# Kernel tuning notes

Measured on AMD Instinct MI355X. Metric: run time of the kernel, lower is better.

Reference implementation:

```python
import jax, jax.numpy as jnp
import numpy as np
import math

D_MODEL = 512
N_HEADS = 8
FACTOR = 5
B, L = 2, 2048


def setup_inputs() -> dict:
    key = jax.random.key(0)
    ks = jax.random.split(key, 10)
    s = 1.0 / math.sqrt(D_MODEL)
    inp = {
        "x": jax.random.normal(ks[0], (B, L, D_MODEL), dtype=jnp.float32),
        "samp_idx": jax.random.randint(ks[1], (FACTOR * L,), 0, L),
        "Wq": jax.random.normal(ks[2], (D_MODEL, D_MODEL), dtype=jnp.float32) * s,
        "bq": jnp.zeros((D_MODEL,), dtype=jnp.float32),
        "Wk": jax.random.normal(ks[3], (D_MODEL, D_MODEL), dtype=jnp.float32) * s,
        "bk": jnp.zeros((D_MODEL,), dtype=jnp.float32),
        "Wv": jax.random.normal(ks[4], (D_MODEL, D_MODEL), dtype=jnp.float32) * s,
        "bv": jnp.zeros((D_MODEL,), dtype=jnp.float32),
        "Wo": jax.random.normal(ks[5], (D_MODEL, D_MODEL), dtype=jnp.float32) * s,
        "bo": jnp.zeros((D_MODEL,), dtype=jnp.float32),
    }
    return inp


def reference(x, Wq, bq, Wk, bk, Wv, bv, Wo, bo, samp_idx):
    B_, L_, D = x.shape
    H = N_HEADS
    dk = D // H
    scale = 1.0 / math.sqrt(dk)

    def proj(W, b):
        # torch Linear: x @ W.T + b, then split heads -> [B, H, L, dk]
        y = jnp.einsum('bld,ed->ble', x, W) + b
        return y.reshape(B_, L_, H, dk).transpose(0, 2, 1, 3)

    q = proj(Wq, bq)
    k = proj(Wk, bk)
    v = proj(Wv, bv)

    # _prob_QK: random key sampling (shared indices across B, H)
    K_sample = k[:, :, samp_idx, :]                       # [B, H, factor*L, dk]
    QKs = jnp.einsum('bhle,bhse->bhls', q, K_sample) * scale  # [B, H, L, factor*L]
    M = QKs.max(-1) - QKs.mean(-1)                        # [B, H, L]
    U = jnp.argmax(M, axis=-1)                            # [B, H] -- single query per head

    # gather the selected query per (b, h): [B, H, 1, dk]
    q_red = jnp.take_along_axis(q, U[:, :, None, None], axis=2)

    scores = jnp.einsum('bhle,bhse->bhls', q_red, k) * scale  # [B, H, 1, L]
    attn = jax.nn.softmax(scores, axis=-1)
    context = jnp.einsum('bhls,bhse->bhle', attn, v)          # [B, H, 1, dk]

    # expand to all query positions, merge heads
    context = jnp.broadcast_to(context, (B_, H, L_, dk))
    context = context.transpose(0, 2, 1, 3).reshape(B_, L_, D)
    return jnp.einsum('bld,ed->ble', context, Wo) + bo
```

## Files before the change

### kernel.cpp

```cpp
#include <hip/hip_runtime.h>

#define B_ 2
#define L_ 2048
#define D_ 512
#define H_ 8
#define DK 64
#define S_ 10240
#define SCALE 0.125f
#define MP_SLICES 16

#define QSZ (4096 * 512)

typedef _Float16 f16;
typedef __attribute__((ext_vector_type(8))) _Float16 f16x8;
typedef __attribute__((ext_vector_type(4))) float f32x4;

__global__ __launch_bounds__(256) void split_x_kernel(
    const float* __restrict__ x, f16* __restrict__ xh, f16* __restrict__ xl)
{
    const size_t i0 = ((size_t)blockIdx.x * 256 + threadIdx.x) * 8;
    const float4 a = *(const float4*)&x[i0];
    const float4 b = *(const float4*)&x[i0 + 4];
    const float vals[8] = {a.x, a.y, a.z, a.w, b.x, b.y, b.z, b.w};
    union { f16 h[8]; uint4 u; } H, Lo;
#pragma unroll
    for (int j = 0; j < 8; j++) {
        const f16 hh = (f16)vals[j];
        H.h[j] = hh;
        Lo.h[j] = (f16)(vals[j] - (float)hh);
    }
    *(uint4*)&xh[i0] = H.u;
    *(uint4*)&xl[i0] = Lo.u;
}

__global__ __launch_bounds__(256) void split_w_kernel(
    const float* __restrict__ Wq, const float* __restrict__ Wk,
    const float* __restrict__ bq, const float* __restrict__ bk,
    f16* __restrict__ wh, f16* __restrict__ wl, float* __restrict__ biascat)
{
    const size_t i0 = ((size_t)blockIdx.x * 256 + threadIdx.x) * 8;
    const float* src = (i0 < (size_t)512 * 512) ? Wq + i0 : Wk + (i0 - (size_t)512 * 512);
    const float4 a = *(const float4*)&src[0];
    const float4 b = *(const float4*)&src[4];
    const float vals[8] = {a.x, a.y, a.z, a.w, b.x, b.y, b.z, b.w};
    union { f16 h[8]; uint4 u; } H, Lo;
#pragma unroll
    for (int j = 0; j < 8; j++) {
        const f16 hh = (f16)vals[j];
        H.h[j] = hh;
        Lo.h[j] = (f16)(vals[j] - (float)hh);
    }
    *(uint4*)&wh[i0] = H.u;
    *(uint4*)&wl[i0] = Lo.u;
    if (blockIdx.x == 0)
        for (int e = threadIdx.x; e < 1024; e += 256)
            biascat[e] = (e < 512) ? bq[e] : bk[e - 512];
}

__global__ __launch_bounds__(256) void projqk_kernel(
    const f16* __restrict__ xh, const f16* __restrict__ xl,
    const f16* __restrict__ wh, const f16* __restrict__ wl,
    const float* __restrict__ biascat,
    f16* __restrict__ qh, f16* __restrict__ ql,
    f16* __restrict__ kh, f16* __restrict__ kl)
{
    const int n0 = blockIdx.x * 128;
    const int e0 = blockIdx.y * 128;
    const int t = threadIdx.x;

    __shared__ __align__(16) f16 lds[4 * 128 * 64];
    f16* ash = lds;
    f16* asl = lds + 8192;
    f16* bsh = lds + 16384;
    f16* bsl = lds + 24576;

    const int lane = t & 63, wid = t >> 6;
    const int wr = wid >> 1, wc = wid & 1;
    const int lrow = lane & 15, lk = lane >> 4;

    f32x4 acc[4][4];
#pragma unroll
    for (int i = 0; i < 4; i++)
#pragma unroll
        for (int j = 0; j < 4; j++)
#pragma unroll
            for (int r = 0; r < 4; r++) acc[i][j][r] = 0.f;

    for (int kt = 0; kt < 8; kt++) {
        __syncthreads();
#pragma unroll
        for (int i = 0; i < 4; i++) {
            const int g = i * 256 + t;
            const int row = g >> 3, c = g & 7;
            const int cs = c ^ (row & 7);
            const int lo = row * 64 + cs * 8;
            const size_t ga = (size_t)(n0 + row) * 512 + kt * 64 + c * 8;
            const size_t gb = (size_t)(e0 + row) * 512 + kt * 64 + c * 8;
            *(uint4*)&ash[lo] = *(const uint4*)&xh[ga];
            *(uint4*)&asl[lo] = *(const uint4*)&xl[ga];
            *(uint4*)&bsh[lo] = *(const uint4*)&wh[gb];
            *(uint4*)&bsl[lo] = *(const uint4*)&wl[gb];
        }
        __syncthreads();

#pragma unroll
        for (int kk = 0; kk < 2; kk++) {
            f16x8 ah[4], al[4], bh_[4], bl_[4];
#pragma unroll
            for (int lt = 0; lt < 4; lt++) {
                const int row = wr * 64 + lt * 16 + lrow;
                const int cs = (kk * 4 + lk) ^ (row & 7);
                const int o = row * 64 + cs * 8;
                ah[lt] = *(const f16x8*)&ash[o];
                al[lt] = *(const f16x8*)&asl[o];
            }
#pragma unroll
            for (int jt = 0; jt < 4; jt++) {
                const int row = wc * 64 + jt * 16 + lrow;
                const int cs = (kk * 4 + lk) ^ (row & 7);
                const int o = row * 64 + cs * 8;
                bh_[jt] = *(const f16x8*)&bsh[o];
                bl_[jt] = *(const f16x8*)&bsl[o];
            }
#pragma unroll
            for (int lt = 0; lt < 4; lt++)
#pragma unroll
                for (int jt = 0; jt < 4; jt++) {
                    acc[lt][jt] = __builtin_amdgcn_mfma_f32_16x16x32_f16(
                        ah[lt], bh_[jt], acc[lt][jt], 0, 0, 0);
                    acc[lt][jt] = __builtin_amdgcn_mfma_f32_16x16x32_f16(
                        ah[lt], bl_[jt], acc[lt][jt], 0, 0, 0);
                    acc[lt][jt] = __builtin_amdgcn_mfma_f32_16x16x32_f16(
                        al[lt], bh_[jt], acc[lt][jt], 0, 0, 0);
                }
        }
    }

    const int PSTR = 72;
    f16* tile = lds + wid * 64 * PSTR;
    const int ebase = e0 + wc * 64;
    const bool isQ = (blockIdx.y < 4);
    const int colbase = (blockIdx.y & 3) * 128;

#pragma unroll
    for (int round = 0; round < 2; round++) {
        __syncthreads();
#pragma unroll
        for (int jt = 0; jt < 4; jt++) {
            const float bval = biascat[ebase + jt * 16 + lrow];
#pragma unroll
            for (int lt = 0; lt < 4; lt++)
#pragma unroll
                for (int r = 0; r < 4; r++) {
                    const float y = acc[lt][jt][r] + bval;
                    const f16 hi = (f16)y;
                    const f16 val = (round == 0) ? hi : (f16)(y - (float)hi);
                    tile[(lt * 16 + lk * 4 + r) * PSTR + jt * 16 + lrow] = val;
                }
        }
        __syncthreads();
        f16* dst = isQ ? ((round == 0) ? qh : ql) : ((round == 0) ? kh : kl);
        for (int i = t; i < 2048; i += 256) {
            const int w = i >> 9, rem = i & 511, row = rem >> 3, c = rem & 7;
            const int n = n0 + (w >> 1) * 64 + row;
            const int col = colbase + (w & 1) * 64 + c * 8;
            *(uint4*)&dst[(size_t)n * 512 + col] =
                *(const uint4*)&lds[w * 64 * PSTR + row * PSTR + c * 8];
        }
    }
}

__global__ void hist_kernel(const int* __restrict__ samp, int* __restrict__ counts)
{
    const int i = blockIdx.x * 256 + threadIdx.x;
    if (i < S_) atomicAdd(&counts[samp[i]], 1);
}

__global__ __launch_bounds__(256) void kbar_part_kernel(
    const f16* __restrict__ kh, const f16* __restrict__ kl,
    const int* __restrict__ counts, float* __restrict__ kbar_part)
{
    const int bh = blockIdx.x, c = blockIdx.y;
    const int b = bh >> 3, h = bh & 7;
    const int j0 = c * 256;
    const int t = threadIdx.x;
    const int e = t & 63, jg = t >> 6;
    const f16* kbh = kh + (size_t)b * L_ * D_ + h * DK + e;
    const f16* kbl = kl + (size_t)b * L_ * D_ + h * DK + e;
    float s = 0.f;
    for (int j = j0 + jg; j < j0 + 256; j += 4) {
        const float kv = (float)kbh[(size_t)j * D_] + (float)kbl[(size_t)j * D_];
        s += (float)counts[j] * kv;
    }
    __shared__ float red[4][64];
    red[jg][e] = s;
    __syncthreads();
    if (t < 64)
        kbar_part[(size_t)(bh * 8 + c) * 64 + t] =
            red[0][t] + red[1][t] + red[2][t] + red[3][t];
}

__global__ __launch_bounds__(256) void mstat_kernel(
    const f16* __restrict__ qh, const f16* __restrict__ ql,
    const f16* __restrict__ kh, const f16* __restrict__ kl,
    const int* __restrict__ counts, float* __restrict__ Mpart)
{
    const int lt16 = blockIdx.x;
    const int bh   = blockIdx.y;
    const int jt16 = blockIdx.z;
    const int b = bh >> 3, h = bh & 7;
    const int l0 = lt16 * 128, j0 = jt16 * 128;
    const int t = threadIdx.x;

    __shared__ __align__(16) f16 qsh[128 * 64];
    __shared__ __align__(16) f16 qsl[128 * 64];
    __shared__ __align__(16) f16 ksh[128 * 64];
    __shared__ __align__(16) f16 ksl[128 * 64];

    {
        const size_t qbase = (size_t)(b * L_ + l0) * D_ + h * DK;
        const size_t kbase = (size_t)(b * L_ + j0) * D_ + h * DK;
#pragma unroll
        for (int i = 0; i < 4; i++) {
            const int g = i * 256 + t;
            const int row = g >> 3, c = g & 7;
            const int cs = c ^ (row & 7);
            const size_t go = (size_t)row * D_ + c * 8;
            const int lo = row * 64 + cs * 8;
            *(uint4*)&qsh[lo] = *(const uint4*)&qh[qbase + go];
            *(uint4*)&qsl[lo] = *(const uint4*)&ql[qbase + go];
            *(uint4*)&ksh[lo] = *(const uint4*)&kh[kbase + go];
            *(uint4*)&ksl[lo] = *(const uint4*)&kl[kbase + go];
        }
    }
    __syncthreads();

    const int lane = t & 63, wid = t >> 6;
    const int wr = wid >> 1, wc = wid & 1;
    const int lrow = lane & 15, lk = lane >> 4;

    f32x4 acc[4][4];
#pragma unroll
    for (int i = 0; i < 4; i++)
#pragma unroll
        for (int j = 0; j < 4; j++)
#pragma unroll
            for (int r = 0; r < 4; r++) acc[i][j][r] = 0.f;

#pragma unroll
    for (int kk = 0; kk < 2; kk++) {
        f16x8 ah[4], al[4], bh_[4], bl_[4];
#pragma unroll
        for (int lt = 0; lt < 4; lt++) {
            const int row = wr * 64 + lt * 16 + lrow;
            const int cs = (kk * 4 + lk) ^ (row & 7);
            const int o = row * 64 + cs * 8;
            ah[lt] = *(const f16x8*)&qsh[o];
            al[lt] = *(const f16x8*)&qsl[o];
        }
#pragma unroll
        for (int jt = 0; jt < 4; jt++) {
            const int row = wc * 64 + jt * 16 + lrow;
            const int cs = (kk * 4 + lk) ^ (row & 7);
            const int o = row * 64 + cs * 8;
            bh_[jt] = *(const f16x8*)&ksh[o];
            bl_[jt] = *(const f16x8*)&ksl[o];
        }
#pragma unroll
        for (int lt = 0; lt < 4; lt++)
#pragma unroll
            for (int jt = 0; jt < 4; jt++) {
                acc[lt][jt] = __builtin_amdgcn_mfma_f32_16x16x32_f16(
                    ah[lt], bh_[jt], acc[lt][jt], 0, 0, 0);
                acc[lt][jt] = __builtin_amdgcn_mfma_f32_16x16x32_f16(
                    ah[lt], bl_[jt], acc[lt][jt], 0, 0, 0);
                acc[lt][jt] = __builtin_amdgcn_mfma_f32_16x16x32_f16(
                    al[lt], bh_[jt], acc[lt][jt], 0, 0, 0);
            }
    }

    float rmax[4][4];
#pragma unroll
    for (int lt = 0; lt < 4; lt++)
#pragma unroll
        for (int r = 0; r < 4; r++) rmax[lt][r] = -3.9e38f;

#pragma unroll
    for (int jt = 0; jt < 4; jt++) {
        const int cj = j0 + wc * 64 + jt * 16 + lrow;
        const float addend = (counts[cj] > 0) ? 0.f : -3.0e38f;
#pragma unroll
        for (int lt = 0; lt < 4; lt++)
#pragma unroll
            for (int r = 0; r < 4; r++)
                rmax[lt][r] = fmaxf(rmax[lt][r], acc[lt][jt][r] + addend);
    }

#pragma unroll
    for (int m = 1; m < 16; m <<= 1)
#pragma unroll
        for (int lt = 0; lt < 4; lt++)
#pragma unroll
            for (int r = 0; r < 4; r++)
                rmax[lt][r] = fmaxf(rmax[lt][r], __shfl_xor(rmax[lt][r], m));

    __syncthreads();
    float* wred = (float*)qsh;
    if (lrow == 0) {
#pragma unroll
        for (int lt = 0; lt < 4; lt++)
#pragma unroll
            for (int r = 0; r < 4; r++)
                wred[wc * 128 + wr * 64 + lt * 16 + lk * 4 + r] = rmax[lt][r];
    }
    __syncthreads();
    if (t < 128)
        Mpart[(size_t)(jt16 * 16 + bh) * L_ + l0 + t] =
            fmaxf(wred[t], wred[128 + t]);
}

__global__ __launch_bounds__(256) void argmax1_kernel(
    const f16* __restrict__ qh, const f16* __restrict__ ql,
    const float* __restrict__ kbar_part, const float* __restrict__ Mpart,
    float* __restrict__ bestv, int* __restrict__ besti)
{
    const int bh = blockIdx.x, c = blockIdx.y;
    const int b = bh >> 3, h = bh & 7;
    const int l0 = c * 256;
    const int t = threadIdx.x;

    __shared__ float kb[64];
    if (t < 64) {
        float s = 0.f;
#pragma unroll
        for (int p = 0; p < 8; p++) s += kbar_part[(size_t)(bh * 8 + p) * 64 + t];
        kb[t] = s * (1.0f / (float)S_);
    }
    __syncthreads();

    const int l = l0 + t;
    const f16* qrh = qh + (size_t)(b * L_ + l) * D_ + h * DK;
    const f16* qrl = ql + (size_t)(b * L_ + l) * D_ + h * DK;
    float dot = 0.f;
#pragma unroll
    for (int cc = 0; cc < 8; cc++) {
        const f16x8 hv = *(const f16x8*)&qrh[cc * 8];
        const f16x8 lv = *(const f16x8*)&qrl[cc * 8];
#pragma unroll
        for (int i = 0; i < 8; i++)
            dot += ((float)hv[i] + (float)lv[i]) * kb[cc * 8 + i];
    }
    float mx = Mpart[(size_t)(0 * 16 + bh) * L_ + l];
#pragma unroll
    for (int p = 1; p < MP_SLICES; p++)
        mx = fmaxf(mx, Mpart[(size_t)(p * 16 + bh) * L_ + l]);
    const float val = mx - dot;

    __shared__ float bvs[256];
    __shared__ int bis[256];
    bvs[t] = val; bis[t] = l;
    __syncthreads();
    for (int s = 128; s > 0; s >>= 1) {
        if (t < s) {
            const float ov = bvs[t + s]; const int oi = bis[t + s];
            if (ov > bvs[t] || (ov == bvs[t] && oi < bis[t])) { bvs[t] = ov; bis[t] = oi; }
        }
        __syncthreads();
    }
    if (t == 0) { bestv[bh * 8 + c] = bvs[0]; besti[bh * 8 + c] = bis[0]; }
}

__global__ void argmax2_kernel(const float* __restrict__ bestv,
                               const int* __restrict__ besti, int* __restrict__ U)
{
    const int t = threadIdx.x;
    if (t < 16) {
        float best = -3.9e38f;
        int bi = 0;
#pragma unroll
        for (int c = 0; c < 8; c++) {
            const float v = bestv[t * 8 + c];
            if (v > best) { best = v; bi = besti[t * 8 + c]; }
        }
        U[t] = bi;
    }
}

__global__ __launch_bounds__(256) void ctx_part_kernel(
    const f16* __restrict__ qh, const f16* __restrict__ ql,
    const f16* __restrict__ kh, const f16* __restrict__ kl,
    const float* __restrict__ x, const int* __restrict__ U,
    float* __restrict__ xbar_part, float* __restrict__ cm, float* __restrict__ cs)
{
    const int bh = blockIdx.x, c = blockIdx.y;
    const int b = bh >> 3, h = bh & 7;
    const int l0 = c * 128;
    const int t = threadIdx.x;

    __shared__ float qr[64];
    __shared__ float w[128];
    __shared__ float red[128];

    const int u = U[bh];
    if (t < 64)
        qr[t] = (float)qh[(size_t)(b * L_ + u) * D_ + h * DK + t] +
                (float)ql[(size_t)(b * L_ + u) * D_ + h * DK + t];
    __syncthreads();

    {
        const int row = t >> 1, half = t & 1;
        const size_t off = (size_t)(b * L_ + l0 + row) * D_ + h * DK + half * 32;
        const f16* krh = kh + off;
        const f16* krl = kl + off;
        float dot = 0.f;
#pragma unroll
        for (int cc = 0; cc < 4; cc++) {
            const f16x8 hv = *(const f16x8*)&krh[cc * 8];
            const f16x8 lv = *(const f16x8*)&krl[cc * 8];
#pragma unroll
            for (int i = 0; i < 8; i++)
                dot += ((float)hv[i] + (float)lv[i]) * qr[half * 32 + cc * 8 + i];
        }
        dot += __shfl_xor(dot, 1);
        if (half == 0) w[row] = dot * SCALE;
    }
    __syncthreads();

    if (t < 128) red[t] = w[t];
    __syncthreads();
    for (int s = 64; s > 0; s >>= 1) {
        if (t < s) red[t] = fmaxf(red[t], red[t + s]);
        __syncthreads();
    }
    const float m = red[0];
    __syncthreads();

    if (t < 128) { const float e = expf(w[t] - m); w[t] = e; red[t] = e; }
    __syncthreads();
    for (int s = 64; s > 0; s >>= 1) {
        if (t < s) red[t] += red[t + s];
        __syncthreads();
    }
    const float ssum = red[0];

    float ax = 0.f, ay = 0.f;
    const float* xb = x + (size_t)(b * L_ + l0) * D_ + t * 2;
#pragma unroll 4
    for (int l = 0; l < 128; l++) {
        const float wl = w[l];
        const float2 xv = *(const float2*)(xb + (size_t)l * D_);
        ax = fmaf(wl, xv.x, ax);
        ay = fmaf(wl, xv.y, ay);
    }
    float2 st; st.x = ax; st.y = ay;
    *(float2*)&xbar_part[(size_t)(bh * 16 + c) * 512 + t * 2] = st;
    if (t == 0) { cm[bh * 16 + c] = m; cs[bh * 16 + c] = ssum; }
}

__global__ __launch_bounds__(256) void ctx_combine_kernel(
    const float* __restrict__ xbar_part, const float* __restrict__ cm,
    const float* __restrict__ cs, const float* __restrict__ Wv,
    const float* __restrict__ bv, float* __restrict__ ctx)
{
    const int bh = blockIdx.x;
    const int h = bh & 7;
    const int t = threadIdx.x;
    __shared__ float xbar[512];

    float M = -3.9e38f;
#pragma unroll
    for (int c = 0; c < 16; c++) M = fmaxf(M, cm[bh * 16 + c]);
    float denom = 0.f;
    float ax = 0.f, ay = 0.f;
#pragma unroll
    for (int c = 0; c < 16; c++) {
        const float f = expf(cm[bh * 16 + c] - M);
        denom += f * cs[bh * 16 + c];
        const float2 p = *(const float2*)&xbar_part[(size_t)(bh * 16 + c) * 512 + t * 2];
        ax = fmaf(f, p.x, ax);
        ay = fmaf(f, p.y, ay);
    }
    xbar[t * 2] = ax; xbar[t * 2 + 1] = ay;
    __syncthreads();

    if (t < 64) {
        const float* wr = Wv + (size_t)(h * 64 + t) * D_;
        float acc = 0.f;
#pragma unroll 8
        for (int d = 0; d < 128; d++) {
            const float4 wv4 = *(const float4*)&wr[d * 4];
            acc += wv4.x * xbar[d * 4] + wv4.y * xbar[d * 4 + 1] +
                   wv4.z * xbar[d * 4 + 2] + wv4.w * xbar[d * 4 + 3];
        }
        ctx[bh * 64 + t] = acc / denom + bv[h * 64 + t];
    }
}

__global__ __launch_bounds__(256) void out_kernel(
    const float* __restrict__ ctx, const float* __restrict__ Wo,
    const float* __restrict__ bo, float* __restrict__ out)
{
    const int b = blockIdx.x;
    const int sl = blockIdx.y;
    const int t = threadIdx.x;
    __shared__ float cb[512];
    __shared__ float row[512];

    cb[t] = ctx[b * 512 + t];
    cb[t + 256] = ctx[b * 512 + 256 + t];
    __syncthreads();

#pragma unroll
    for (int r = 0; r < 2; r++) {
        const int e = t + r * 256;
        const float* wr = Wo + (size_t)e * D_;
        float acc = 0.f;
#pragma unroll 8
        for (int c = 0; c < 128; c++) {
            const float4 wv = *(const float4*)(wr + c * 4);
            acc += wv.x * cb[c * 4] + wv.y * cb[c * 4 + 1] +
                   wv.z * cb[c * 4 + 2] + wv.w * cb[c * 4 + 3];
        }
        row[e] = acc + bo[e];
    }
    __syncthreads();

    const float4* r4 = (const float4*)row;
    float4* o4 = (float4*)(out + ((size_t)b * L_ + sl * 32) * D_);
    for (int i = t; i < 32 * 128; i += 256) {
        const int l = i >> 7, c = i & 127;
        o4[l * 128 + c] = r4[c];
    }
}

extern "C" void kernel_launch(void* const* d_in, const int* in_sizes, int n_in,
                              void* d_out, int out_size, void* d_ws, size_t ws_size,
                              hipStream_t stream)
{
    const float* x   = (const float*)d_in[0];
    const int* samp  = (const int*)d_in[1];
    const float* Wq  = (const float*)d_in[2];
    const float* bq  = (const float*)d_in[3];
    const float* Wk  = (const float*)d_in[4];
    const float* bk  = (const float*)d_in[5];
    const float* Wv  = (const float*)d_in[6];
    const float* bv  = (const float*)d_in[7];
    const float* Wo  = (const float*)d_in[8];
    const float* bo  = (const float*)d_in[9];
    float* out = (float*)d_out;

    f16* qh = (f16*)d_ws;
    f16* ql = qh + QSZ;
    f16* kh = ql + QSZ;
    f16* kl = kh + QSZ;
    f16* xh = kl + QSZ;
    f16* xl = xh + QSZ;
    f16* wh = xl + QSZ;
    f16* wl = wh + 1024 * 512;
    float* fbase     = (float*)(wl + 1024 * 512);
    float* biascat   = fbase;
    float* Mpart     = biascat + 1024;
    float* kbar_part = Mpart + MP_SLICES * 16 * L_;
    float* xbar_part = kbar_part + 8192;
    float* cm        = xbar_part + 131072;
    float* cs        = cm + 256;
    float* bestv     = cs + 256;
    float* ctx       = bestv + 128;
    int* counts      = (int*)(ctx + 1024);
    int* besti       = counts + 2048;
    int* U           = besti + 128;

    hipMemsetAsync(counts, 0, 2048 * sizeof(int), stream);
    split_x_kernel<<<1024, 256, 0, stream>>>(x, xh, xl);
    split_w_kernel<<<256, 256, 0, stream>>>(Wq, Wk, bq, bk, wh, wl, biascat);
    projqk_kernel<<<dim3(32, 8), 256, 0, stream>>>(xh, xl, wh, wl, biascat,
                                                   qh, ql, kh, kl);
    hist_kernel<<<40, 256, 0, stream>>>(samp, counts);
    kbar_part_kernel<<<dim3(16, 8), 256, 0, stream>>>(kh, kl, counts, kbar_part);
    mstat_kernel<<<dim3(16, 16, 16), 256, 0, stream>>>(qh, ql, kh, kl, counts, Mpart);
    argmax1_kernel<<<dim3(16, 8), 256, 0, stream>>>(qh, ql, kbar_part, Mpart, bestv, besti);
    argmax2_kernel<<<1, 64, 0, stream>>>(bestv, besti, U);
    ctx_part_kernel<<<dim3(16, 16), 256, 0, stream>>>(qh, ql, kh, kl, x, U,
                                                      xbar_part, cm, cs);
    ctx_combine_kernel<<<16, 256, 0, stream>>>(xbar_part, cm, cs, Wv, bv, ctx);
    out_kernel<<<dim3(2, 64), 256, 0, stream>>>(ctx, Wo, bo, out);
}
```

Before: 164.8 us.

## Fuse M-statistic and argmax into persistent-over-keys mstat kernel with double-buffered K tiles

The mstat kernel now has each block loop over all 16 key tiles, with double-buffered LDS staging. It keeps the query fragments in registers and folds the max reduction, the kbar dot product and the per-block argmax into the same kernel. This removes the Mpart global round trip, the argmax1 kernel and the j-slice grid dimension, and it remaps block IDs so blocks for the same head land on the same XCD. The output stage is split into a tiny row-compute kernel and a wide broadcast kernel, so the Wo matvec is no longer repeated 64 times. The trade-off is that the grid drops from 4096 blocks to 256 longer-running blocks and two extra launches are added.

Result: slower. 206.0 us (+25.0%).

```diff
diff --git a/kernel.cpp b/kernel.cpp
--- a/kernel.cpp
+++ b/kernel.cpp
@@ -7,7 +7,6 @@
 #define DK 64
 #define S_ 10240
 #define SCALE 0.125f
-#define MP_SLICES 16
 
 #define QSZ (4096 * 512)
 
@@ -200,84 +199,76 @@
             red[0][t] + red[1][t] + red[2][t] + red[3][t];
 }
 
+__global__ void kbar_combine_kernel(const float* __restrict__ kbar_part,
+                                    float* __restrict__ kbar)
+{
+    const int bh = blockIdx.x;
+    const int t = threadIdx.x;
+    float s = 0.f;
+#pragma unroll
+    for (int p = 0; p < 8; p++) s += kbar_part[(size_t)(bh * 8 + p) * 64 + t];
+    kbar[bh * 64 + t] = s * (1.0f / (float)S_);
+}
+
 __global__ __launch_bounds__(256) void mstat_kernel(
     const f16* __restrict__ qh, const f16* __restrict__ ql,
     const f16* __restrict__ kh, const f16* __restrict__ kl,
-    const int* __restrict__ counts, float* __restrict__ Mpart)
-{
-    const int lt16 = blockIdx.x;
-    const int bh   = blockIdx.y;
-    const int jt16 = blockIdx.z;
+    const int* __restrict__ counts, const float* __restrict__ kbar,
+    float* __restrict__ bestv, int* __restrict__ besti)
+{
+    const int id = blockIdx.x;
+    const int xcd = id & 7, seq = id >> 3;
+    const int bh = xcd * 2 + (seq >> 4);
+    const int lt16 = seq & 15;
     const int b = bh >> 3, h = bh & 7;
-    const int l0 = lt16 * 128, j0 = jt16 * 128;
-    const int t = threadIdx.x;
-
-    __shared__ __align__(16) f16 qsh[128 * 64];
-    __shared__ __align__(16) f16 qsl[128 * 64];
-    __shared__ __align__(16) f16 ksh[128 * 64];
-    __shared__ __align__(16) f16 ksl[128 * 64];
-
-    {
-        const size_t qbase = (size_t)(b * L_ + l0) * D_ + h * DK;
-        const size_t kbase = (size_t)(b * L_ + j0) * D_ + h * DK;
-#pragma unroll
-        for (int i = 0; i < 4; i++) {
-            const int g = i * 256 + t;
-            const int row = g >> 3, c = g & 7;
-            const int cs = c ^ (row & 7);
-            const size_t go = (size_t)row * D_ + c * 8;
-            const int lo = row * 64 + cs * 8;
-            *(uint4*)&qsh[lo] = *(const uint4*)&qh[qbase + go];
-            *(uint4*)&qsl[lo] = *(const uint4*)&ql[qbase + go];
-            *(uint4*)&ksh[lo] = *(const uint4*)&kh[kbase + go];
-            *(uint4*)&ksl[lo] = *(const uint4*)&kl[kbase + go];
-        }
-    }
-    __syncthreads();
-
+    const int l0 = lt16 * 128;
+    const int t = threadIdx.x;
     const int lane = t & 63, wid = t >> 6;
     const int wr = wid >> 1, wc = wid & 1;
     const int lrow = lane & 15, lk = lane >> 4;
 
-    f32x4 acc[4][4];
-#pragma unroll
-    for (int i = 0; i < 4; i++)
-#pragma unroll
-        for (int j = 0; j < 4; j++)
-#pragma unroll
-            for (int r = 0; r < 4; r++) acc[i][j][r] = 0.f;
-
-#pragma unroll
-    for (int kk = 0; kk < 2; kk++) {
-        f16x8 ah[4], al[4], bh_[4], bl_[4];
-#pragma unroll
-        for (int lt = 0; lt < 4; lt++) {
-            const int row = wr * 64 + lt * 16 + lrow;
-            const int cs = (kk * 4 + lk) ^ (row & 7);
-            const int o = row * 64 + cs * 8;
-            ah[lt] = *(const f16x8*)&qsh[o];
-            al[lt] = *(const f16x8*)&qsl[o];
-        }
-#pragma unroll
-        for (int jt = 0; jt < 4; jt++) {
-            const int row = wc * 64 + jt * 16 + lrow;
-            const int cs = (kk * 4 + lk) ^ (row & 7);
-            const int o = row * 64 + cs * 8;
-            bh_[jt] = *(const f16x8*)&ksh[o];
-            bl_[jt] = *(const f16x8*)&ksl[o];
-        }
-#pragma unroll
-        for (int lt = 0; lt < 4; lt++)
-#pragma unroll
-            for (int jt = 0; jt < 4; jt++) {
-                acc[lt][jt] = __builtin_amdgcn_mfma_f32_16x16x32_f16(
-                    ah[lt], bh_[jt], acc[lt][jt], 0, 0, 0);
-                acc[lt][jt] = __builtin_amdgcn_mfma_f32_16x16x32_f16(
-                    ah[lt], bl_[jt], acc[lt][jt], 0, 0, 0);
-                acc[lt][jt] = __builtin_amdgcn_mfma_f32_16x16x32_f16(
-                    al[lt], bh_[jt], acc[lt][jt], 0, 0, 0);
+    __shared__ __align__(16) f16 kbuf[2][2][128 * 64];
+    __shared__ float kbar_lds[64];
+    __shared__ float dot_lds[128];
+    __shared__ float wv_[4];
+    __shared__ int wi_[4];
+
+    f16x8 qa_h[2][4], qa_l[2][4];
+    {
+        const size_t qrowbase = (size_t)(b * L_ + l0 + wr * 64) * D_ + h * DK;
+#pragma unroll
+        for (int kk = 0; kk < 2; kk++)
+#pragma unroll
+            for (int lt = 0; lt < 4; lt++) {
+                const size_t o = qrowbase + (size_t)(lt * 16 + lrow) * D_ + kk * 32 + lk * 8;
+                qa_h[kk][lt] = *(const f16x8*)&qh[o];
+                qa_l[kk][lt] = *(const f16x8*)&ql[o];
             }
     }
+    if (t < 64) kbar_lds[t] = kbar[bh * 64 + t];
+
+    const f16* khb = kh + (size_t)b * L_ * D_ + h * DK;
+    const f16* klb = kl + (size_t)b * L_ * D_ + h * DK;
+
+    const int srow = t >> 3, sc = t & 7;
+    (void)srow; (void)sc;
+
+    uint4 rh[4], rl[4];
+#pragma unroll
+    for (int i = 0; i < 4; i++) {
+        const int g = i * 256 + t, row = g >> 3, c = g & 7;
+        const size_t go = (size_t)row * D_ + c * 8;
+        rh[i] = *(const uint4*)&khb[go];
+        rl[i] = *(const uint4*)&klb[go];
+    }
+#pragma unroll
+    for (int i = 0; i < 4; i++) {
+        const int g = i * 256 + t, row = g >> 3, c = g & 7;
+        const int cs = c ^ (row & 7);
+        *(uint4*)&kbuf[0][0][row * 64 + cs * 8] = rh[i];
+        *(uint4*)&kbuf[0][1][row * 64 + cs * 8] = rl[i];
+    }
+    __syncthreads();
 
     float rmax[4][4];
 #pragma unroll
@@ -285,15 +276,74 @@
 #pragma unroll
         for (int r = 0; r < 4; r++) rmax[lt][r] = -3.9e38f;
 
-#pragma unroll
-    for (int jt = 0; jt < 4; jt++) {
-        const int cj = j0 + wc * 64 + jt * 16 + lrow;
-        const float addend = (counts[cj] > 0) ? 0.f : -3.0e38f;
-#pragma unroll
-        for (int lt = 0; lt < 4; lt++)
-#pragma unroll
-            for (int r = 0; r < 4; r++)
-                rmax[lt][r] = fmaxf(rmax[lt][r], acc[lt][jt][r] + addend);
+    int cur = 0;
+    for (int jt = 0; jt < 16; jt++) {
+        if (jt < 15) {
+            const size_t kbase = (size_t)((jt + 1) * 128) * D_;
+#pragma unroll
+            for (int i = 0; i < 4; i++) {
+                const int g = i * 256 + t, row = g >> 3, c = g & 7;
+                const size_t go = kbase + (size_t)row * D_ + c * 8;
+                rh[i] = *(const uint4*)&khb[go];
+                rl[i] = *(const uint4*)&klb[go];
+            }
+        }
+
+        f32x4 acc[4][4];
+#pragma unroll
+        for (int i = 0; i < 4; i++)
+#pragma unroll
+            for (int j = 0; j < 4; j++)
+#pragma unroll
+                for (int r = 0; r < 4; r++) acc[i][j][r] = 0.f;
+
+#pragma unroll
+        for (int kk = 0; kk < 2; kk++) {
+            f16x8 bhf[4], blf[4];
+#pragma unroll
+            for (int jtt = 0; jtt < 4; jtt++) {
+                const int row = wc * 64 + jtt * 16 + lrow;
+                const int cs = (kk * 4 + lk) ^ (row & 7);
+                const int o = row * 64 + cs * 8;
+                bhf[jtt] = *(const f16x8*)&kbuf[cur][0][o];
+                blf[jtt] = *(const f16x8*)&kbuf[cur][1][o];
+            }
+#pragma unroll
+            for (int lt = 0; lt < 4; lt++)
+#pragma unroll
+                for (int jtt = 0; jtt < 4; jtt++) {
+                    acc[lt][jtt] = __builtin_amdgcn_mfma_f32_16x16x32_f16(
+                        qa_h[kk][lt], bhf[jtt], acc[lt][jtt], 0, 0, 0);
+                    acc[lt][jtt] = __builtin_amdgcn_mfma_f32_16x16x32_f16(
+                        qa_h[kk][lt], blf[jtt], acc[lt][jtt], 0, 0, 0);
+                    acc[lt][jtt] = __builtin_amdgcn_mfma_f32_16x16x32_f16(
+                        qa_l[kk][lt], bhf[jtt], acc[lt][jtt], 0, 0, 0);
+                }
+        }
+
+#pragma unroll
+        for (int jtt = 0; jtt < 4; jtt++) {
+            const int cj = jt * 128 + wc * 64 + jtt * 16 + lrow;
+            const float addend = (counts[cj] > 0) ? 0.f : -3.0e38f;
+#pragma unroll
+            for (int lt = 0; lt < 4; lt++)
+#pragma unroll
+                for (int r = 0; r < 4; r++)
+                    rmax[lt][r] = fmaxf(rmax[lt][r], acc[lt][jtt][r] + addend);
+        }
+
+        __syncthreads();
+        if (jt < 15) {
+#pragma unroll
+            for (int i = 0; i < 4; i++) {
+                const int g = i * 256 + t, row = g >> 3, c = g & 7;
+                const int cs = c ^ (row & 7);
+                *(uint4*)&kbuf[cur ^ 1][0][row * 64 + cs * 8] = rh[i];
+                *(uint4*)&kbuf[cur ^ 1][1][row * 64 + cs * 8] = rl[i];
+            }
+        }
+        __syncthreads();
+        cur ^= 1;
     }
 
 #pragma unroll
@@ -304,70 +354,62 @@
             for (int r = 0; r < 4; r++)
                 rmax[lt][r] = fmaxf(rmax[lt][r], __shfl_xor(rmax[lt][r], m));
 
-    __syncthreads();
-    float* wred = (float*)qsh;
-    if (lrow == 0) {
-#pragma unroll
-        for (int lt = 0; lt < 4; lt++)
-#pragma unroll
-            for (int r = 0; r < 4; r++)
-                wred[wc * 128 + wr * 64 + lt * 16 + lk * 4 + r] = rmax[lt][r];
-    }
-    __syncthreads();
-    if (t < 128)
-        Mpart[(size_t)(jt16 * 16 + bh) * L_ + l0 + t] =
-            fmaxf(wred[t], wred[128 + t]);
-}
-
-__global__ __launch_bounds__(256) void argmax1_kernel(
-    const f16* __restrict__ qh, const f16* __restrict__ ql,
-    const float* __restrict__ kbar_part, const float* __restrict__ Mpart,
-    float* __restrict__ bestv, int* __restrict__ besti)
-{
-    const int bh = blockIdx.x, c = blockIdx.y;
-    const int b = bh >> 3, h = bh & 7;
-    const int l0 = c * 256;
-    const int t = threadIdx.x;
-
-    __shared__ float kb[64];
-    if (t < 64) {
-        float s = 0.f;
-#pragma unroll
-        for (int p = 0; p < 8; p++) s += kbar_part[(size_t)(bh * 8 + p) * 64 + t];
-        kb[t] = s * (1.0f / (float)S_);
-    }
-    __syncthreads();
-
-    const int l = l0 + t;
-    const f16* qrh = qh + (size_t)(b * L_ + l) * D_ + h * DK;
-    const f16* qrl = ql + (size_t)(b * L_ + l) * D_ + h * DK;
-    float dot = 0.f;
-#pragma unroll
-    for (int cc = 0; cc < 8; cc++) {
-        const f16x8 hv = *(const f16x8*)&qrh[cc * 8];
-        const f16x8 lv = *(const f16x8*)&qrl[cc * 8];
-#pragma unroll
-        for (int i = 0; i < 8; i++)
-            dot += ((float)hv[i] + (float)lv[i]) * kb[cc * 8 + i];
-    }
-    float mx = Mpart[(size_t)(0 * 16 + bh) * L_ + l];
-#pragma unroll
-    for (int p = 1; p < MP_SLICES; p++)
-        mx = fmaxf(mx, Mpart[(size_t)(p * 16 + bh) * L_ + l]);
-    const float val = mx - dot;
-
-    __shared__ float bvs[256];
-    __shared__ int bis[256];
-    bvs[t] = val; bis[t] = l;
-    __syncthreads();
-    for (int s = 128; s > 0; s >>= 1) {
-        if (t < s) {
-            const float ov = bvs[t + s]; const int oi = bis[t + s];
-            if (ov > bvs[t] || (ov == bvs[t] && oi < bis[t])) { bvs[t] = ov; bis[t] = oi; }
-        }
-        __syncthreads();
-    }
-    if (t == 0) { bestv[bh * 8 + c] = bvs[0]; besti[bh * 8 + c] = bis[0]; }
+    {
+        float dlt[4];
+#pragma unroll
+        for (int lt = 0; lt < 4; lt++) {
+            float d = 0.f;
+#pragma unroll
+            for (int kk = 0; kk < 2; kk++) {
+                const f16x8 hv = qa_h[kk][lt];
+                const f16x8 lv = qa_l[kk][lt];
+#pragma unroll
+                for (int i = 0; i < 8; i++)
+                    d += ((float)hv[i] + (float)lv[i]) * kbar_lds[kk * 32 + lk * 8 + i];
+            }
+            dlt[lt] = d;
+        }
+#pragma unroll
+        for (int lt = 0; lt < 4; lt++) {
+            dlt[lt] += __shfl_xor(dlt[lt], 16);
+            dlt[lt] += __shfl_xor(dlt[lt], 32);
+        }
+        if (lane < 16) {
+#pragma unroll
+            for (int lt = 0; lt < 4; lt++)
+                dot_lds[wr * 64 + lt * 16 + lane] = dlt[lt];
+        }
+    }
+    __syncthreads();
+
+    float bv_ = -3.9e38f;
+    int bi_ = 0x7fffffff;
+#pragma unroll
+    for (int lt = 0; lt < 4; lt++)
+#pragma unroll
+        for (int r = 0; r < 4; r++) {
+            const int rl_ = wr * 64 + lt * 16 + lk * 4 + r;
+            const float val = rmax[lt][r] - dot_lds[rl_];
+            const int idx = l0 + rl_;
+            if (val > bv_ || (val == bv_ && idx < bi_)) { bv_ = val; bi_ = idx; }
+        }
+#pragma unroll
+    for (int m = 1; m < 64; m <<= 1) {
+        const float ov = __shfl_xor(bv_, m);
+        const int oi = __shfl_xor(bi_, m);
+        if (ov > bv_ || (ov == bv_ && oi < bi_)) { bv_ = ov; bi_ = oi; }
+    }
+    if (lane == 0) { wv_[wid] = bv_; wi_[wid] = bi_; }
+    __syncthreads();
+    if (t == 0) {
+        float fb = wv_[0]; int fi = wi_[0];
+#pragma unroll
+        for (int w = 1; w < 4; w++) {
+            if (wv_[w] > fb || (wv_[w] == fb && wi_[w] < fi)) { fb = wv_[w]; fi = wi_[w]; }
+        }
+        bestv[bh * 16 + lt16] = fb;
+        besti[bh * 16 + lt16] = fi;
+    }
 }
 
 __global__ void argmax2_kernel(const float* __restrict__ bestv,
@@ -378,9 +420,10 @@
         float best = -3.9e38f;
         int bi = 0;
 #pragma unroll
-        for (int c = 0; c < 8; c++) {
-            const float v = bestv[t * 8 + c];
-            if (v > best) { best = v; bi = besti[t * 8 + c]; }
+        for (int c = 0; c < 16; c++) {
+            const float v = bestv[t * 16 + c];
+            const int oi = besti[t * 16 + c];
+            if (v > best || (v == best && oi < bi)) { best = v; bi = oi; }
         }
         U[t] = bi;
     }
@@ -496,20 +539,16 @@
     }
 }
 
-__global__ __launch_bounds__(256) void out_kernel(
+__global__ __launch_bounds__(256) void out_row_kernel(
     const float* __restrict__ ctx, const float* __restrict__ Wo,
-    const float* __restrict__ bo, float* __restrict__ out)
+    const float* __restrict__ bo, float* __restrict__ rowbuf)
 {
     const int b = blockIdx.x;
-    const int sl = blockIdx.y;
     const int t = threadIdx.x;
     __shared__ float cb[512];
-    __shared__ float row[512];
-
     cb[t] = ctx[b * 512 + t];
     cb[t + 256] = ctx[b * 512 + 256 + t];
     __syncthreads();
-
 #pragma unroll
     for (int r = 0; r < 2; r++) {
         const int e = t + r * 256;
@@ -521,16 +560,17 @@
             acc += wv.x * cb[c * 4] + wv.y * cb[c * 4 + 1] +
                    wv.z * cb[c * 4 + 2] + wv.w * cb[c * 4 + 3];
         }
-        row[e] = acc + bo[e];
-    }
-    __syncthreads();
-
-    const float4* r4 = (const float4*)row;
-    float4* o4 = (float4*)(out + ((size_t)b * L_ + sl * 32) * D_);
-    for (int i = t; i < 32 * 128; i += 256) {
-        const int l = i >> 7, c = i & 127;
-        o4[l * 128 + c] = r4[c];
-    }
+        rowbuf[b * 512 + e] = acc + bo[e];
+    }
+}
+
+__global__ __launch_bounds__(256) void out_bcast_kernel(
+    const float* __restrict__ rowbuf, float* __restrict__ out)
+{
+    const int g = blockIdx.x * 256 + threadIdx.x;
+    const int l = g >> 7, c = g & 127;
+    const int b = l >> 11;
+    ((float4*)out)[g] = ((const float4*)rowbuf)[b * 128 + c];
 }
 
 extern "C" void kernel_launch(void* const* d_in, const int* in_sizes, int n_in,
@@ -559,16 +599,17 @@
     f16* wl = wh + 1024 * 512;
     float* fbase     = (float*)(wl + 1024 * 512);
     float* biascat   = fbase;
-    float* Mpart     = biascat + 1024;
-    float* kbar_part = Mpart + MP_SLICES * 16 * L_;
-    float* xbar_part = kbar_part + 8192;
+    float* kbar_part = biascat + 1024;
+    float* kbar      = kbar_part + 8192;
+    float* xbar_part = kbar + 1024;
     float* cm        = xbar_part + 131072;
     float* cs        = cm + 256;
     float* bestv     = cs + 256;
-    float* ctx       = bestv + 128;
-    int* counts      = (int*)(ctx + 1024);
+    float* ctx       = bestv + 256;
+    float* rowbuf    = ctx + 1024;
+    int* counts      = (int*)(rowbuf + 1024);
     int* besti       = counts + 2048;
-    int* U           = besti + 128;
+    int* U           = besti + 256;
 
     hipMemsetAsync(counts, 0, 2048 * sizeof(int), stream);
     split_x_kernel<<<1024, 256, 0, stream>>>(x, xh, xl);
@@ -577,11 +618,12 @@
                                                    qh, ql, kh, kl);
     hist_kernel<<<40, 256, 0, stream>>>(samp, counts);
     kbar_part_kernel<<<dim3(16, 8), 256, 0, stream>>>(kh, kl, counts, kbar_part);
-    mstat_kernel<<<dim3(16, 16, 16), 256, 0, stream>>>(qh, ql, kh, kl, counts, Mpart);
-    argmax1_kernel<<<dim3(16, 8), 256, 0, stream>>>(qh, ql, kbar_part, Mpart, bestv, besti);
+    kbar_combine_kernel<<<16, 64, 0, stream>>>(kbar_part, kbar);
+    mstat_kernel<<<256, 256, 0, stream>>>(qh, ql, kh, kl, counts, kbar, bestv, besti);
     argmax2_kernel<<<1, 64, 0, stream>>>(bestv, besti, U);
     ctx_part_kernel<<<dim3(16, 16), 256, 0, stream>>>(qh, ql, kh, kl, x, U,
                                                       xbar_part, cm, cs);
     ctx_combine_kernel<<<16, 256, 0, stream>>>(xbar_part, cm, cs, Wv, bv, ctx);
-    out_kernel<<<dim3(2, 64), 256, 0, stream>>>(ctx, Wo, bo, out);
-}
+    out_row_kernel<<<2, 256, 0, stream>>>(ctx, Wo, bo, rowbuf);
+    out_bcast_kernel<<<2048, 256, 0, stream>>>(rowbuf, out);
+}
```
